# Performance work log

Hardware: AMD Instinct MI355X
Metric: run time of the kernel (lower is better)

The kernel has to match this reference:

```python
import jax, jax.numpy as jnp
import numpy as np

N, T = 4096, 1024
COND, PRED, PERIOD = 896, 56, 7


def setup_inputs() -> dict:
    key = jax.random.key(0)
    k1, k2 = jax.random.split(key)
    query = jax.random.normal(k1, (N, T), dtype=jnp.float32)
    # learned per-location params: [init_level, level_sm_logit, init_trend,
    #  trend_sm_logit, season_sm, period seasonality logits]
    params = 0.1 * jax.random.normal(k2, (N, 5 + PERIOD), dtype=jnp.float32)
    return {"query": query, "params": params}


def _forward(query, params):
    init_level = params[:, 0]                       # [N]
    level_sm = jax.nn.sigmoid(params[:, 1])         # [N]
    init_trend = params[:, 2]                       # [N]
    trend_sm = jax.nn.sigmoid(params[:, 3])         # [N]
    season_sm = params[:, 4]                        # NOTE: no sigmoid, matches original code
    init_seas = jax.nn.sigmoid(params[:, -PERIOD:])  # [N, PERIOD]

    def step(carry, y):
        prev_level, prev_trend, buf = carry          # buf: rolling window of last PERIOD seasonalities
        s_t = buf[:, 0]                              # seasonalities[t]
        pred = prev_level + prev_trend
        level = level_sm * y + (1.0 - level_sm) * pred
        diff = jnp.abs(level - prev_level)
        trend = trend_sm * (level - prev_level) + (1.0 - trend_sm) * prev_trend
        new_seas = season_sm * (y - pred) + (1.0 - season_sm) * s_t
        buf = jnp.concatenate([buf[:, 1:], new_seas[:, None]], axis=1)
        return (level, trend, buf), (level, trend, new_seas, diff)

    carry0 = (init_level, init_trend, init_seas)
    _, (levels, trends, new_seas_seq, diffs) = jax.lax.scan(step, carry0, query.T)
    levels = levels.T            # [N, T]
    trends = trends.T            # [N, T]
    new_seas_seq = new_seas_seq.T  # [N, T], == seasonalities[:, PERIOD:]
    level_diffs = diffs.T.mean(axis=1)  # [N]

    # full seasonality sequence: PERIOD initial values followed by T computed ones
    seas_full = jnp.concatenate([init_seas, new_seas_seq], axis=1)  # [N, PERIOD+T]

    sm = query - levels - new_seas_seq  # [N, T]

    horizon = jnp.arange(1, PRED + 1, dtype=levels.dtype)  # [PRED]
    last_levels = levels[:, COND - 1:, None]   # [N, W, 1], W = T-COND+1
    last_trends = trends[:, COND - 1:, None]
    pr = last_levels + last_trends * horizon   # [N, W, PRED]

    # cyclic seasonality forecast per window
    season_index = jnp.tile(jnp.arange(PERIOD), (PRED + PERIOD - 1) // PERIOD)[:PRED]
    starts = jnp.arange(COND, T + 1)           # [W]
    idx = starts[:, None] + season_index[None, :]  # [W, PRED]
    pr = pr + seas_full[:, idx]                # [N, W, PRED]

    return sm, pr, level_diffs


def reference(query, params):
    return _forward(query, params)
```

## Files before the change

### kernel.cpp

```cpp
#include <hip/hip_runtime.h>
#include <cmath>

#define NROWS 4096
#define TLEN  1024
#define RPB   8
#define LT0   895
#define ST0   889
#define LTN   129
#define STN   135
#define PRV4R 1806
#define PRV4B (RPB * PRV4R)

__device__ __forceinline__ float sigmoidf_(float x) {
    return 1.0f / (1.0f + expf(-x));
}

__device__ __forceinline__ float f4c(const float4& v, int k) {
    switch (k & 3) { case 0: return v.x; case 1: return v.y; case 2: return v.z; default: return v.w; }
}

__global__ __launch_bounds__(256, 2)
void es_fused(const float* __restrict__ query,
              const float* __restrict__ params,
              float* __restrict__ sm,
              float* __restrict__ diffs,
              float4* __restrict__ pr4)
{
    __shared__ float4 ystage[RPB * 256];
    __shared__ float lds_P[RPB * 65];
    __shared__ float lds_start[RPB * 65];
    __shared__ float lds_q[RPB * 225];
    __shared__ float lds_dsum[RPB * 33];
    __shared__ float lds_par[RPB * 16];
    __shared__ float Ltl[RPB * 132];
    __shared__ float Ttl[RPB * 132];
    __shared__ float Stl[RPB * 136];

    const int tid = threadIdx.x;
    const int r = tid >> 5;
    const int k = tid & 31;
    const int base = blockIdx.x * RPB;
    const int n = base + r;

    {
        const float4* qb = reinterpret_cast<const float4*>(query + (size_t)base * TLEN);
        const int cs = tid ^ ((tid >> 3) & 7);
        #pragma unroll
        for (int i = 0; i < 8; ++i)
            ystage[i * 256 + cs] = qb[i * 256 + tid];
    }

    const float* pp = params + (size_t)n * 12;
    const float a  = sigmoidf_(pp[1]);
    const float b  = sigmoidf_(pp[3]);
    const float c  = pp[4];
    const float ia = 1.0f - a, ib = 1.0f - b, ic = 1.0f - c;

    __syncthreads();

    float4 yv[8];
    {
        const int ksw = k & 7;
        #pragma unroll
        for (int i = 0; i < 8; ++i)
            yv[i] = ystage[r * 256 + ((k * 8 + i) ^ ksw)];
    }

    {
        float L = 0.0f, B = 0.0f;
        #pragma unroll
        for (int j = 0; j < 32; ++j) {
            const float yy = f4c(yv[j >> 2], j);
            const float pred  = L + B;
            const float level = fmaf(a, yy, ia * pred);
            const float trend = fmaf(b, level - L, ib * B);
            L = level; B = trend;
        }
        lds_P[r * 65 + 2 * k]     = L;
        lds_P[r * 65 + 2 * k + 1] = B;
    }
    if (k == 0) {
        float* par = &lds_par[r * 16];
        par[0] = pp[0];
        par[1] = pp[2];
        par[2] = ia;
        par[3] = -(a * b);
        par[4] = ib + b * ia;
        par[5] = ic;
        #pragma unroll
        for (int l = 0; l < 7; ++l) par[6 + l] = sigmoidf_(pp[5 + l]);
    }
    __syncthreads();

    if (tid < 8) {
        const float* par = &lds_par[tid * 16];
        float m00 = par[2], m01 = par[2], m10 = par[3], m11 = par[4];
        #pragma unroll
        for (int s = 0; s < 5; ++s) {
            const float t00 = m00 * m00 + m01 * m10;
            const float t01 = m00 * m01 + m01 * m11;
            const float t10 = m10 * m00 + m11 * m10;
            const float t11 = m10 * m01 + m11 * m11;
            m00 = t00; m01 = t01; m10 = t10; m11 = t11;
        }
        float P0[32], P1[32];
        #pragma unroll
        for (int kk = 0; kk < 32; ++kk) {
            P0[kk] = lds_P[tid * 65 + 2 * kk];
            P1[kk] = lds_P[tid * 65 + 2 * kk + 1];
        }
        float s0 = par[0], s1 = par[1];
        #pragma unroll
        for (int kk = 0; kk < 32; ++kk) {
            lds_start[tid * 65 + 2 * kk]     = s0;
            lds_start[tid * 65 + 2 * kk + 1] = s1;
            const float t0 = m00 * s0 + m01 * s1 + P0[kk];
            const float t1 = m10 * s0 + m11 * s1 + P1[kk];
            s0 = t0; s1 = t1;
        }
    }
    __syncthreads();

    const float st0 = lds_start[r * 65 + 2 * k];
    const float st1 = lds_start[r * 65 + 2 * k + 1];

    float e[32];
    {
        float L = st0, B = st1, dsum = 0.0f;
        float q[7] = {0,0,0,0,0,0,0};
        #pragma unroll
        for (int j = 0; j < 32; ++j) {
            const float yy = f4c(yv[j >> 2], j);
            const float pred  = L + B;
            const float level = fmaf(a, yy, ia * pred);
            const float d     = level - L;
            dsum += fabsf(d);
            const float trend = fmaf(b, d, ib * B);
            const float ee    = yy - pred;
            e[j] = ee;
            q[j % 7] = fmaf(ic, q[j % 7], c * ee);
            L = level; B = trend;
        }
        const int kp = (4 * k) % 7;
        #pragma unroll
        for (int l = 0; l < 7; ++l) {
            int g = kp + l; if (g >= 7) g -= 7;
            lds_q[r * 225 + k * 7 + g] = q[l];
        }
        lds_dsum[r * 33 + k] = dsum;
    }

    if (k >= 27) {
        float prevL = st0, Bv = st1;
        #pragma unroll
        for (int j = 0; j < 32; ++j) {
            const float level = f4c(yv[j >> 2], j) - ia * e[j];
            const float trend = fmaf(b, level - prevL, ib * Bv);
            const int tg = k * 32 + j;
            if (tg >= LT0) {
                Ltl[r * 132 + tg - LT0] = level;
                Ttl[r * 132 + tg - LT0] = trend;
            }
            prevL = level; Bv = trend;
        }
    }
    __syncthreads();

    if (tid < 56) {
        const int rr = tid / 7, p = tid % 7;
        const float icc = lds_par[rr * 16 + 5];
        const float ic2 = icc * icc;
        const float ic4 = ic2 * ic2;
        const float ic5 = ic4 * icc;
        float v = lds_par[rr * 16 + 6 + p];
        float qq[32];
        #pragma unroll
        for (int kk = 0; kk < 32; ++kk) qq[kk] = lds_q[rr * 225 + kk * 7 + p];
        int l = p;
        #pragma unroll
        for (int kk = 0; kk < 32; ++kk) {
            const float m = (l < 4) ? ic5 : ic4;
            const float nv = fmaf(m, v, qq[kk]);
            lds_q[rr * 225 + kk * 7 + p] = v;
            v = nv;
            l += 3; if (l >= 7) l -= 7;
        }
    } else if (tid < 64) {
        const int rr = tid - 56;
        float s = 0.0f;
        #pragma unroll
        for (int kk = 0; kk < 32; ++kk) s += lds_dsum[rr * 33 + kk];
        diffs[blockIdx.x * RPB + rr] = s * (1.0f / 1024.0f);
    }
    __syncthreads();

    {
        float sg[7];
        const int kp = (4 * k) % 7;
        #pragma unroll
        for (int l = 0; l < 7; ++l) {
            int g = kp + l; if (g >= 7) g -= 7;
            sg[l] = lds_q[r * 225 + k * 7 + g];
        }
        const int ksw = k & 7;
        float4 ov;
        #pragma unroll
        for (int j = 0; j < 32; ++j) {
            const float sn = fmaf(ic, sg[j % 7], c * e[j]);
            sg[j % 7] = sn;
            const float smv = ia * e[j] - sn;
            e[j] = sn;
            switch (j & 3) { case 0: ov.x = smv; break; case 1: ov.y = smv; break;
                             case 2: ov.z = smv; break; default: ov.w = smv; }
            if ((j & 3) == 3)
                ystage[r * 256 + ((k * 8 + (j >> 2)) ^ ksw)] = ov;
        }
        if (k >= 27) {
            #pragma unroll
            for (int j = 0; j < 32; ++j) {
                const int tg = k * 32 + j;
                if (tg >= ST0) Stl[r * 136 + tg - ST0] = e[j];
            }
        }
    }
    __syncthreads();

    {
        float4* smb = reinterpret_cast<float4*>(sm + (size_t)base * TLEN);
        const int cs = tid ^ ((tid >> 3) & 7);
        #pragma unroll
        for (int i = 0; i < 8; ++i)
            smb[i * 256 + tid] = ystage[i * 256 + cs];
    }

    {
        float4* prb = pr4 + (size_t)blockIdx.x * PRV4B;
        int row = 0;
        int s   = tid / 14;
        int h4  = tid - s * 14;
        int m0  = (4 * h4) % 7;
        for (int i = 0; i < 57; ++i) {
            const int q = i * 256 + tid;
            if (q < PRV4B) {
                const float L = Ltl[row * 132 + s];
                const float T = Ttl[row * 132 + s];
                const float* stp = &Stl[row * 136 + s];
                int m1 = m0 + 1; if (m1 >= 7) m1 -= 7;
                int m2 = m1 + 1; if (m2 >= 7) m2 -= 7;
                int m3 = m2 + 1; if (m3 >= 7) m3 -= 7;
                const float hb = (float)(h4 * 4);
                float4 o;
                o.x = fmaf(T, hb + 1.0f, L) + stp[m0];
                o.y = fmaf(T, hb + 2.0f, L) + stp[m1];
                o.z = fmaf(T, hb + 3.0f, L) + stp[m2];
                o.w = fmaf(T, hb + 4.0f, L) + stp[m3];
                prb[q] = o;
            }
            h4 += 4; s += 18;
            if (h4 >= 14) { h4 -= 14; s += 1; }
            if (s >= 129) { s -= 129; row += 1; }
            m0 += 2; if (m0 >= 7) m0 -= 7;
        }
    }
}

extern "C" void kernel_launch(void* const* d_in, const int* in_sizes, int n_in,
                              void* d_out, int out_size, void* d_ws, size_t ws_size,
                              hipStream_t stream) {
    const float* query  = (const float*)d_in[0];
    const float* params = (const float*)d_in[1];

    float* out   = (float*)d_out;
    float* sm    = out;
    float* pr    = out + (size_t)NROWS * TLEN;
    float* diffs = pr  + (size_t)NROWS * 129 * 56;

    hipLaunchKernelGGL(es_fused, dim3(NROWS / RPB), dim3(256), 0, stream,
                       query, params, sm, diffs, (float4*)pr);
}
```

Baseline: 35.74 us.

## Double block size so extra waves share the staging and forecast stores

Launches 512 threads per block instead of 256. Only the first 256 threads run the per-row scan phases, and all 512 share the global load and store of the staged series and the large forecast-output write loop. The forecast loop now computes its indices directly by division instead of carrying incremental counters. The intent is more memory-level parallelism on the store-heavy tail, at the cost of idle waves during the scan phases and a tighter register budget from the higher occupancy bound.

New measurement: 34.77 us. -2.7%, faster.

```diff
diff --git a/kernel.cpp b/kernel.cpp
--- a/kernel.cpp
+++ b/kernel.cpp
@@ -19,7 +19,7 @@
     switch (k & 3) { case 0: return v.x; case 1: return v.y; case 2: return v.z; default: return v.w; }
 }
 
-__global__ __launch_bounds__(256, 2)
+__global__ __launch_bounds__(512, 4)
 void es_fused(const float* __restrict__ query,
               const float* __restrict__ params,
               float* __restrict__ sm,
@@ -37,36 +37,51 @@
     __shared__ float Stl[RPB * 136];
 
     const int tid = threadIdx.x;
-    const int r = tid >> 5;
+    const int base = blockIdx.x * RPB;
+    const int r = (tid >> 5) & 7;
     const int k = tid & 31;
-    const int base = blockIdx.x * RPB;
     const int n = base + r;
 
     {
         const float4* qb = reinterpret_cast<const float4*>(query + (size_t)base * TLEN);
-        const int cs = tid ^ ((tid >> 3) & 7);
-        #pragma unroll
-        for (int i = 0; i < 8; ++i)
-            ystage[i * 256 + cs] = qb[i * 256 + tid];
-    }
-
-    const float* pp = params + (size_t)n * 12;
-    const float a  = sigmoidf_(pp[1]);
-    const float b  = sigmoidf_(pp[3]);
-    const float c  = pp[4];
-    const float ia = 1.0f - a, ib = 1.0f - b, ic = 1.0f - c;
-
+        #pragma unroll
+        for (int i = 0; i < 4; ++i) {
+            const int w = i * 512 + tid;
+            ystage[(w & ~7) | ((w ^ (w >> 3)) & 7)] = qb[w];
+        }
+    }
+
+    float a = 0.f, b = 0.f, c = 0.f, ia = 0.f, ib = 0.f, ic = 0.f;
+    if (tid < 256) {
+        const float* pp = params + (size_t)n * 12;
+        a  = sigmoidf_(pp[1]);
+        b  = sigmoidf_(pp[3]);
+        c  = pp[4];
+        ia = 1.0f - a; ib = 1.0f - b; ic = 1.0f - c;
+        if (k == 0) {
+            float* par = &lds_par[r * 16];
+            par[0] = pp[0];
+            par[1] = pp[2];
+            par[2] = ia;
+            par[3] = -(a * b);
+            par[4] = ib + b * ia;
+            par[5] = ic;
+            #pragma unroll
+            for (int l = 0; l < 7; ++l) par[6 + l] = sigmoidf_(pp[5 + l]);
+        }
+    }
     __syncthreads();
 
     float4 yv[8];
-    {
+    float e[32];
+    float st0 = 0.f, st1 = 0.f;
+
+    if (tid < 256) {
         const int ksw = k & 7;
         #pragma unroll
         for (int i = 0; i < 8; ++i)
             yv[i] = ystage[r * 256 + ((k * 8 + i) ^ ksw)];
-    }
-
-    {
+
         float L = 0.0f, B = 0.0f;
         #pragma unroll
         for (int j = 0; j < 32; ++j) {
@@ -79,17 +94,6 @@
         lds_P[r * 65 + 2 * k]     = L;
         lds_P[r * 65 + 2 * k + 1] = B;
     }
-    if (k == 0) {
-        float* par = &lds_par[r * 16];
-        par[0] = pp[0];
-        par[1] = pp[2];
-        par[2] = ia;
-        par[3] = -(a * b);
-        par[4] = ib + b * ia;
-        par[5] = ic;
-        #pragma unroll
-        for (int l = 0; l < 7; ++l) par[6 + l] = sigmoidf_(pp[5 + l]);
-    }
     __syncthreads();
 
     if (tid < 8) {
@@ -121,11 +125,9 @@
     }
     __syncthreads();
 
-    const float st0 = lds_start[r * 65 + 2 * k];
-    const float st1 = lds_start[r * 65 + 2 * k + 1];
-
-    float e[32];
-    {
+    if (tid < 256) {
+        st0 = lds_start[r * 65 + 2 * k];
+        st1 = lds_start[r * 65 + 2 * k + 1];
         float L = st0, B = st1, dsum = 0.0f;
         float q[7] = {0,0,0,0,0,0,0};
         #pragma unroll
@@ -148,20 +150,20 @@
             lds_q[r * 225 + k * 7 + g] = q[l];
         }
         lds_dsum[r * 33 + k] = dsum;
-    }
-
-    if (k >= 27) {
-        float prevL = st0, Bv = st1;
-        #pragma unroll
-        for (int j = 0; j < 32; ++j) {
-            const float level = f4c(yv[j >> 2], j) - ia * e[j];
-            const float trend = fmaf(b, level - prevL, ib * Bv);
-            const int tg = k * 32 + j;
-            if (tg >= LT0) {
-                Ltl[r * 132 + tg - LT0] = level;
-                Ttl[r * 132 + tg - LT0] = trend;
+
+        if (k >= 27) {
+            float prevL = st0, Bv = st1;
+            #pragma unroll
+            for (int j = 0; j < 32; ++j) {
+                const float level = f4c(yv[j >> 2], j) - ia * e[j];
+                const float trend = fmaf(b, level - prevL, ib * Bv);
+                const int tg = k * 32 + j;
+                if (tg >= LT0) {
+                    Ltl[r * 132 + tg - LT0] = level;
+                    Ttl[r * 132 + tg - LT0] = trend;
+                }
+                prevL = level; Bv = trend;
             }
-            prevL = level; Bv = trend;
         }
     }
     __syncthreads();
@@ -194,7 +196,7 @@
     }
     __syncthreads();
 
-    {
+    if (tid < 256) {
         float sg[7];
         const int kp = (4 * k) % 7;
         #pragma unroll
@@ -227,39 +229,59 @@
 
     {
         float4* smb = reinterpret_cast<float4*>(sm + (size_t)base * TLEN);
-        const int cs = tid ^ ((tid >> 3) & 7);
-        #pragma unroll
-        for (int i = 0; i < 8; ++i)
-            smb[i * 256 + tid] = ystage[i * 256 + cs];
+        #pragma unroll
+        for (int i = 0; i < 4; ++i) {
+            const int w = i * 512 + tid;
+            smb[w] = ystage[(w & ~7) | ((w ^ (w >> 3)) & 7)];
+        }
     }
 
     {
         float4* prb = pr4 + (size_t)blockIdx.x * PRV4B;
-        int row = 0;
-        int s   = tid / 14;
-        int h4  = tid - s * 14;
-        int m0  = (4 * h4) % 7;
-        for (int i = 0; i < 57; ++i) {
-            const int q = i * 256 + tid;
-            if (q < PRV4B) {
-                const float L = Ltl[row * 132 + s];
-                const float T = Ttl[row * 132 + s];
-                const float* stp = &Stl[row * 136 + s];
-                int m1 = m0 + 1; if (m1 >= 7) m1 -= 7;
-                int m2 = m1 + 1; if (m2 >= 7) m2 -= 7;
-                int m3 = m2 + 1; if (m3 >= 7) m3 -= 7;
-                const float hb = (float)(h4 * 4);
-                float4 o;
-                o.x = fmaf(T, hb + 1.0f, L) + stp[m0];
-                o.y = fmaf(T, hb + 2.0f, L) + stp[m1];
-                o.z = fmaf(T, hb + 3.0f, L) + stp[m2];
-                o.w = fmaf(T, hb + 4.0f, L) + stp[m3];
-                prb[q] = o;
-            }
-            h4 += 4; s += 18;
-            if (h4 >= 14) { h4 -= 14; s += 1; }
-            if (s >= 129) { s -= 129; row += 1; }
-            m0 += 2; if (m0 >= 7) m0 -= 7;
+        #pragma unroll 4
+        for (int i = 0; i < 28; ++i) {
+            const int q = i * 512 + tid;
+            const int row = q / PRV4R;
+            const int rem = q - row * PRV4R;
+            const int s   = rem / 14;
+            const int h4  = rem - s * 14;
+            const float L = Ltl[row * 132 + s];
+            const float T = Ttl[row * 132 + s];
+            const float* stp = &Stl[row * 136 + s];
+            const int hb = h4 * 4;
+            int m0 = hb % 7;
+            int m1 = m0 + 1; if (m1 >= 7) m1 -= 7;
+            int m2 = m1 + 1; if (m2 >= 7) m2 -= 7;
+            int m3 = m2 + 1; if (m3 >= 7) m3 -= 7;
+            const float hbf = (float)hb;
+            float4 o;
+            o.x = fmaf(T, hbf + 1.0f, L) + stp[m0];
+            o.y = fmaf(T, hbf + 2.0f, L) + stp[m1];
+            o.z = fmaf(T, hbf + 3.0f, L) + stp[m2];
+            o.w = fmaf(T, hbf + 4.0f, L) + stp[m3];
+            prb[q] = o;
+        }
+        const int q = 28 * 512 + tid;
+        if (q < PRV4B) {
+            const int row = q / PRV4R;
+            const int rem = q - row * PRV4R;
+            const int s   = rem / 14;
+            const int h4  = rem - s * 14;
+            const float L = Ltl[row * 132 + s];
+            const float T = Ttl[row * 132 + s];
+            const float* stp = &Stl[row * 136 + s];
+            const int hb = h4 * 4;
+            int m0 = hb % 7;
+            int m1 = m0 + 1; if (m1 >= 7) m1 -= 7;
+            int m2 = m1 + 1; if (m2 >= 7) m2 -= 7;
+            int m3 = m2 + 1; if (m3 >= 7) m3 -= 7;
+            const float hbf = (float)hb;
+            float4 o;
+            o.x = fmaf(T, hbf + 1.0f, L) + stp[m0];
+            o.y = fmaf(T, hbf + 2.0f, L) + stp[m1];
+            o.z = fmaf(T, hbf + 3.0f, L) + stp[m2];
+            o.w = fmaf(T, hbf + 4.0f, L) + stp[m3];
+            prb[q] = o;
         }
     }
 }
@@ -275,6 +297,6 @@
     float* pr    = out + (size_t)NROWS * TLEN;
     float* diffs = pr  + (size_t)NROWS * 129 * 56;
 
-    hipLaunchKernelGGL(es_fused, dim3(NROWS / RPB), dim3(256), 0, stream,
+    hipLaunchKernelGGL(es_fused, dim3(NROWS / RPB), dim3(512), 0, stream,
                        query, params, sm, diffs, (float4*)pr);
 }
```
